# Kernel tuning notes

Measured on AMD Instinct MI355X. Metric: run time of the kernel, lower is better.

Reference implementation:

```python
import jax, jax.numpy as jnp
import numpy as np

B, T, D = 2, 2048, 1024
H, K = 16, 64  # num_heads, key_size (value_size == key_size)


def setup_inputs() -> dict:
    key = jax.random.key(0)
    ks = jax.random.split(key, 9)
    # xavier-uniform-ish scale for square-ish projections
    def xavier(k, shape):
        fan_in, fan_out = shape[0], shape[1]
        lim = jnp.sqrt(6.0 / (fan_in + fan_out))
        return jax.random.uniform(k, shape, jnp.float32, -lim, lim)
    return {
        "x_q": jax.random.normal(ks[0], (B, T, D), jnp.float32),
        "Wq": xavier(ks[1], (D, H * K)),
        "bq": jnp.zeros((H * K,), jnp.float32),
        "Wk": xavier(ks[2], (D, H * K)),
        "bk": jnp.zeros((H * K,), jnp.float32),
        "Wv": xavier(ks[3], (D, H * K)),
        "bv": jnp.zeros((H * K,), jnp.float32),
        "Wo": xavier(ks[4], (H * K, D)),
        "bo": jnp.zeros((D,), jnp.float32),
    }


def reference(x_q, Wq, bq, Wk, bk, Wv, bv, Wo, bo):
    # self-attention: x_k = x_v = x_q
    q = (x_q @ Wq + bq).reshape(B, T, H, K)
    k = (x_q @ Wk + bk).reshape(B, T, H, K)
    v = (x_q @ Wv + bv).reshape(B, T, H, K)
    # dense_dot_product_attention, mask=None
    logits = jnp.einsum('bqhd,bkhd->bhqk', q, k) / jnp.sqrt(jnp.asarray(K, k.dtype))
    attn_w = jax.nn.softmax(logits, axis=-1)  # [B,H,Tq,Tk]
    attn = jnp.einsum('bhqk,bkhd->bqhd', attn_w, v).reshape(B, T, H * K)
    out = attn @ Wo + bo  # [B,T,D]
    return out
```

## Files before the change

kernel.cpp:

```cpp
#include <hip/hip_runtime.h>
#include <hip/hip_bf16.h>
#include <stdint.h>

#define B_  2
#define T_  2048
#define D_  1024
#define H_  16
#define KS  64
#define M_  (B_*T_)

typedef unsigned short u16;
typedef __bf16 bf16x8 __attribute__((ext_vector_type(8)));
typedef __bf16 bf16x4 __attribute__((ext_vector_type(4)));
typedef float  f32x4  __attribute__((ext_vector_type(4)));

#define AS1 __attribute__((address_space(1)))
#define AS3 __attribute__((address_space(3)))

__device__ inline u16 f2bf(float x){
  union { float f; uint32_t u; } v; v.f = x;
  uint32_t r = (v.u + 0x7fffu + ((v.u >> 16) & 1u)) >> 16;
  return (u16)r;
}

__device__ inline void gl_lds16(const u16* g, u16* l){
  __builtin_amdgcn_global_load_lds((AS1 void*)(const_cast<u16*>(g)),
                                   (AS3 void*)l, 16, 0, 0);
}

__global__ __launch_bounds__(256) void k_cvt_x(const float* __restrict__ x,
                                               u16* __restrict__ xb){
  int i = blockIdx.x * 256 + threadIdx.x;
  float4 v = ((const float4*)x)[i];
  ushort4 o;
  o.x = f2bf(v.x); o.y = f2bf(v.y); o.z = f2bf(v.z); o.w = f2bf(v.w);
  ((ushort4*)xb)[i] = o;
}

__global__ __launch_bounds__(256) void k_tconv_w(const float* __restrict__ W0,
                                                 const float* __restrict__ W1,
                                                 const float* __restrict__ W2,
                                                 const float* __restrict__ W3,
                                                 u16* __restrict__ out){
  const float* W = (blockIdx.z==0)?W0:(blockIdx.z==1)?W1:(blockIdx.z==2)?W2:W3;
  u16* o = out + (size_t)blockIdx.z * 1024 * 1024;
  __shared__ float tile[32][33];
  int tx = threadIdx.x, ty = threadIdx.y;
  int kb = blockIdx.y * 32, nb = blockIdx.x * 32;
  for(int i=0;i<4;i++) tile[ty+8*i][tx] = W[(size_t)(kb+ty+8*i)*1024 + nb+tx];
  __syncthreads();
  for(int i=0;i<4;i++){
    int n = nb + ty + 8*i;
    o[(size_t)n*1024 + kb + tx] = f2bf(tile[tx][ty+8*i]);
  }
}

__global__ __launch_bounds__(256) void k_gemm_qkv(const u16* __restrict__ xb,
                                                  const u16* __restrict__ wt,
                                                  const float* __restrict__ bq,
                                                  const float* __restrict__ bk,
                                                  const float* __restrict__ bv,
                                                  u16* __restrict__ qkv){
  int widx = blockIdx.x >> 3;
  int n0   = (blockIdx.x & 7) * 128;
  int m0   = blockIdx.y * 128;
  const u16* BT = wt + (size_t)widx * (1024*1024);
  const float* bias = (widx==0)?bq:(widx==1)?bk:bv;
  u16* out = qkv + (size_t)widx * (4*1024*1024);
  float oscale = (widx==0) ? 0.125f * 1.44269504088896f : 1.0f;

  __shared__ u16 Asm[128*64];
  __shared__ u16 Bsm[128*64];
  int t = threadIdx.x;
  int lane = t & 63, w = t >> 6, wm = w >> 1, wn = w & 1;
  int l15 = lane & 15, l4 = lane >> 4;
  f32x4 zero = {0.f,0.f,0.f,0.f};
  f32x4 acc[4][4];
  for(int i=0;i<4;i++) for(int j=0;j<4;j++) acc[i][j] = zero;
  int srow = t >> 3, schunk = t & 7;

  for(int kt=0; kt<16; ++kt){
    __syncthreads();
    int kb = kt * 64;
    for(int i=0;i<4;i++){
      int row = i*32 + srow;
      int gch = schunk ^ (row & 7);
      gl_lds16(xb + (size_t)(m0+row)*1024 + kb + gch*8, Asm + row*64 + schunk*8);
      gl_lds16(BT + (size_t)(n0+row)*1024 + kb + gch*8, Bsm + row*64 + schunk*8);
    }
    __syncthreads();
    for(int c=0;c<2;c++){
      bf16x8 af[4], bfr[4];
      for(int mt=0;mt<4;mt++){
        int row = wm*64 + mt*16 + l15;
        int idx = (row*64 + c*32 + l4*8) ^ ((row & 7) << 3);
        af[mt] = *(const bf16x8*)(Asm + idx);
      }
      for(int nt=0;nt<4;nt++){
        int row = wn*64 + nt*16 + l15;
        int idx = (row*64 + c*32 + l4*8) ^ ((row & 7) << 3);
        bfr[nt] = *(const bf16x8*)(Bsm + idx);
      }
      for(int mt=0;mt<4;mt++)
        for(int nt=0;nt<4;nt++)
          acc[mt][nt] = __builtin_amdgcn_mfma_f32_16x16x32_bf16(af[mt], bfr[nt], acc[mt][nt], 0,0,0);
    }
  }
  for(int nt=0;nt<4;nt++){
    int nbase = n0 + wn*64 + nt*16 + l15;
    float bv_ = bias[nbase];
    int h = nbase >> 6, kk = nbase & 63;
    for(int mt=0;mt<4;mt++){
      for(int r=0;r<4;r++){
        int m = m0 + wm*64 + mt*16 + l4*4 + r;
        int b = m >> 11, tt = m & 2047;
        out[(((size_t)(b*H_ + h)*T_ + tt) << 6) + kk] = f2bf((acc[mt][nt][r] + bv_) * oscale);
      }
    }
  }
}

__global__ __launch_bounds__(256) void k_tpose_v(const u16* __restrict__ V,
                                                 u16* __restrict__ VT){
  __shared__ u16 tile[64][65];
  int bh = blockIdx.y, tt = blockIdx.x;
  const u16* v = V + ((size_t)bh*T_ + (size_t)tt*64) * 64;
  u16* o = VT + (size_t)bh*64*T_ + (size_t)tt*64;
  int t = threadIdx.x;
  for(int i=0;i<2;i++){
    int r = i*32 + (t>>3); int c0 = (t&7)*8;
    bf16x8 d = *(const bf16x8*)(v + (size_t)r*64 + c0);
    for(int j=0;j<8;j++) tile[r][c0+j] = ((u16*)&d)[j];
  }
  __syncthreads();
  for(int i=0;i<2;i++){
    int d0 = i*32 + (t>>3); int c0 = (t&7)*8;
    union { u16 s[8]; uint4 q; } pk;
    for(int j=0;j<8;j++) pk.s[j] = tile[c0+j][d0];
    *(uint4*)(o + (size_t)d0*T_ + c0) = pk.q;
  }
}

__global__ __launch_bounds__(256) void k_attn(const u16* __restrict__ Q,
                                              const u16* __restrict__ Kg,
                                              const u16* __restrict__ VT,
                                              u16* __restrict__ attn_out){
  int bx = blockIdx.x;
  int qt = bx & 31, h = (bx >> 5) & 15, b = bx >> 9;
  int bh = b*H_ + h;
  const u16* Qh = Q  + (size_t)bh * T_ * 64;
  const u16* Kh = Kg + (size_t)bh * T_ * 64;
  const u16* Vh = VT + (size_t)bh * 64 * T_;
  __shared__ u16 Ksm[2][64*64];
  __shared__ u16 Vsm[2][64*64];
  __shared__ u16 Psm[4][16*64];
  int t = threadIdx.x, lane = t & 63, w = t >> 6;
  int l15 = lane & 15, l4 = lane >> 4;

  bf16x8 qf[2];
  int qrow = qt*64 + w*16 + l15;
  for(int c=0;c<2;c++)
    qf[c] = *(const bf16x8*)(Qh + (size_t)qrow*64 + c*32 + l4*8);

  f32x4 zero = {0.f,0.f,0.f,0.f};
  f32x4 accT[4];
  for(int g=0;g<4;g++) accT[g] = zero;
  float m_r = -3.0e38f, l_r = 0.f;

  int srow = t >> 3, schunk = t & 7;

  for(int i=0;i<2;i++){
    int row = i*32 + srow;
    int gch = schunk ^ (row & 7);
    gl_lds16(Kh + (size_t)row*64 + gch*8,  &Ksm[0][row*64 + schunk*8]);
    gl_lds16(Vh + (size_t)row*T_ + gch*8,  &Vsm[0][row*64 + schunk*8]);
  }
  __syncthreads();

  int cur = 0;
  for(int tile=0; tile<32; ++tile){
    if(tile+1 < 32){
      int kvb = (tile+1)*64;
      for(int i=0;i<2;i++){
        int row = i*32 + srow;
        int gch = schunk ^ (row & 7);
        gl_lds16(Kh + (size_t)(kvb+row)*64 + gch*8, &Ksm[cur^1][row*64 + schunk*8]);
        gl_lds16(Vh + (size_t)row*T_ + kvb + gch*8, &Vsm[cur^1][row*64 + schunk*8]);
      }
    }

    f32x4 s[4];
    for(int g=0;g<4;g++) s[g] = zero;
    __builtin_amdgcn_s_setprio(1);
    for(int c=0;c<2;c++){
      for(int g=0;g<4;g++){
        int row = g*16 + l15;
        int idx = (row*64 + c*32 + l4*8) ^ ((row & 7) << 3);
        bf16x8 kf = *(const bf16x8*)(&Ksm[cur][idx]);
        s[g] = __builtin_amdgcn_mfma_f32_16x16x32_bf16(kf, qf[c], s[g], 0,0,0);
      }
    }
    __builtin_amdgcn_s_setprio(0);

    float pmax = s[0][0];
    for(int g=0;g<4;g++)
      for(int r=0;r<4;r++) pmax = fmaxf(pmax, s[g][r]);
    pmax = fmaxf(pmax, __shfl_xor(pmax, 16));
    pmax = fmaxf(pmax, __shfl_xor(pmax, 32));
    if(__any(pmax > m_r + 8.f)){
      float mnew  = fmaxf(m_r, pmax);
      float alpha = __builtin_amdgcn_exp2f(m_r - mnew);
      m_r = mnew;
      l_r *= alpha;
      for(int g=0;g<4;g++){
        f32x4 a = accT[g];
        for(int r=0;r<4;r++) a[r] *= alpha;
        accT[g] = a;
      }
    }
    float rs = 0.f;
    for(int g=0;g<4;g++)
      for(int r=0;r<4;r++){
        float e = __builtin_amdgcn_exp2f(s[g][r] - m_r);
        s[g][r] = e;
        rs += e;
      }
    rs += __shfl_xor(rs, 16);
    rs += __shfl_xor(rs, 32);
    l_r += rs;

    for(int g=0;g<4;g++){
      bf16x4 pk;
      for(int r=0;r<4;r++) pk[r] = (__bf16)s[g][r];
      int idx = (l15*64 + g*16 + l4*4) ^ ((l15 & 7) << 3);
      *(bf16x4*)(&Psm[w][idx]) = pk;
    }

    __builtin_amdgcn_s_setprio(1);
    for(int c=0;c<2;c++){
      int idx_p = (l15*64 + c*32 + l4*8) ^ ((l15 & 7) << 3);
      bf16x8 pf = *(const bf16x8*)(&Psm[w][idx_p]);
      for(int g=0;g<4;g++){
        int row = g*16 + l15;
        int idx = (row*64 + c*32 + l4*8) ^ ((row & 7) << 3);
        bf16x8 vf = *(const bf16x8*)(&Vsm[cur][idx]);
        accT[g] = __builtin_amdgcn_mfma_f32_16x16x32_bf16(vf, pf, accT[g], 0,0,0);
      }
    }
    __builtin_amdgcn_s_setprio(0);

    __syncthreads();
    cur ^= 1;
  }

  float oinv = 1.0f / l_r;
  int m = b*T_ + qt*64 + w*16 + l15;
  for(int g=0;g<4;g++){
    bf16x4 pk;
    for(int r=0;r<4;r++) pk[r] = (__bf16)(accT[g][r] * oinv);
    *(bf16x4*)(attn_out + (size_t)m*1024 + h*64 + g*16 + l4*4) = pk;
  }
}

__global__ __launch_bounds__(256) void k_gemm_out(const u16* __restrict__ A,
                                                  const u16* __restrict__ BT,
                                                  const float* __restrict__ bias,
                                                  float* __restrict__ out){
  int n0 = blockIdx.x * 128;
  int m0 = blockIdx.y * 64;
  __shared__ u16 Asm[64*64];
  __shared__ u16 Bsm[128*64];
  int t = threadIdx.x;
  int lane = t & 63, w = t >> 6, wm = w >> 1, wn = w & 1;
  int l15 = lane & 15, l4 = lane >> 4;
  f32x4 zero = {0.f,0.f,0.f,0.f};
  f32x4 acc[2][4];
  for(int i=0;i<2;i++) for(int j=0;j<4;j++) acc[i][j] = zero;
  int srow = t >> 3, schunk = t & 7;

  for(int kt=0; kt<16; ++kt){
    __syncthreads();
    int kb = kt * 64;
    for(int i=0;i<2;i++){
      int row = i*32 + srow;
      int gch = schunk ^ (row & 7);
      gl_lds16(A  + (size_t)(m0+row)*1024 + kb + gch*8, Asm + row*64 + schunk*8);
    }
    for(int i=0;i<4;i++){
      int row = i*32 + srow;
      int gch = schunk ^ (row & 7);
      gl_lds16(BT + (size_t)(n0+row)*1024 + kb + gch*8, Bsm + row*64 + schunk*8);
    }
    __syncthreads();
    for(int c=0;c<2;c++){
      bf16x8 af[2], bfr[4];
      for(int mt=0;mt<2;mt++){
        int row = wm*32 + mt*16 + l15;
        int idx = (row*64 + c*32 + l4*8) ^ ((row & 7) << 3);
        af[mt] = *(const bf16x8*)(Asm + idx);
      }
      for(int nt=0;nt<4;nt++){
        int row = wn*64 + nt*16 + l15;
        int idx = (row*64 + c*32 + l4*8) ^ ((row & 7) << 3);
        bfr[nt] = *(const bf16x8*)(Bsm + idx);
      }
      for(int mt=0;mt<2;mt++)
        for(int nt=0;nt<4;nt++)
          acc[mt][nt] = __builtin_amdgcn_mfma_f32_16x16x32_bf16(af[mt], bfr[nt], acc[mt][nt], 0,0,0);
    }
  }
  for(int nt=0;nt<4;nt++){
    int nbase = n0 + wn*64 + nt*16 + l15;
    float bv_ = bias[nbase];
    for(int mt=0;mt<2;mt++){
      for(int r=0;r<4;r++){
        int m = m0 + wm*32 + mt*16 + l4*4 + r;
        out[(size_t)m*1024 + nbase] = acc[mt][nt][r] + bv_;
      }
    }
  }
}

extern "C" void kernel_launch(void* const* d_in, const int* in_sizes, int n_in,
                              void* d_out, int out_size, void* d_ws, size_t ws_size,
                              hipStream_t stream){
  const float* x  = (const float*)d_in[0];
  const float* Wq = (const float*)d_in[1];
  const float* bq = (const float*)d_in[2];
  const float* Wk = (const float*)d_in[3];
  const float* bk = (const float*)d_in[4];
  const float* Wv = (const float*)d_in[5];
  const float* bv = (const float*)d_in[6];
  const float* Wo = (const float*)d_in[7];
  const float* bo = (const float*)d_in[8];
  float* out = (float*)d_out;
  char* ws = (char*)d_ws;

  u16* xb  = (u16*)(ws);
  u16* wt  = (u16*)(ws + (8u  << 20));
  u16* qkv = (u16*)(ws + (16u << 20));
  u16* vt  = (u16*)(ws + (40u << 20));
  u16* at  = (u16*)(ws + (48u << 20));

  k_cvt_x   <<<4096, 256, 0, stream>>>(x, xb);
  k_tconv_w <<<dim3(32,32,4), dim3(32,8), 0, stream>>>(Wq, Wk, Wv, Wo, wt);
  k_gemm_qkv<<<dim3(24,32), 256, 0, stream>>>(xb, wt, bq, bk, bv, qkv);
  k_tpose_v <<<dim3(32,32), 256, 0, stream>>>(qkv + (size_t)8*1024*1024, vt);
  k_attn    <<<1024, 256, 0, stream>>>(qkv, qkv + (size_t)4*1024*1024, vt, at);
  k_gemm_out<<<dim3(8,64), 256, 0, stream>>>(at, wt + (size_t)3*1024*1024, bo, out);
}
```

Before: 219.5 us.

## Fuse V transpose into QKV GEMM epilogue and compute softmax row sums via MFMA

The QKV GEMM now writes V directly in transposed [bh][d][t] layout with 4-wide packed stores, which removes the separate k_tpose_v kernel launch and its extra read and write of V. In the attention kernel, the per-tile row sum of exponentials is computed by an extra MFMA of a ones vector against the P fragment instead of scalar adds plus cross-lane shuffles. The rescaling of the sum moves into the accumulator, and the row max reduction is rebalanced into a tree. Costs are one extra MFMA per chunk, and the sum is taken from bf16-rounded P, which slightly changes numerics.

Measured after the change: 212.8 us. 3.0% less time.

```diff
diff --git a/kernel.cpp b/kernel.cpp
--- a/kernel.cpp
+++ b/kernel.cpp
@@ -60,7 +60,8 @@
                                                   const float* __restrict__ bq,
                                                   const float* __restrict__ bk,
                                                   const float* __restrict__ bv,
-                                                  u16* __restrict__ qkv){
+                                                  u16* __restrict__ qkv,
+                                                  u16* __restrict__ vt){
   int widx = blockIdx.x >> 3;
   int n0   = (blockIdx.x & 7) * 128;
   int m0   = blockIdx.y * 128;
@@ -106,38 +107,32 @@
           acc[mt][nt] = __builtin_amdgcn_mfma_f32_16x16x32_bf16(af[mt], bfr[nt], acc[mt][nt], 0,0,0);
     }
   }
-  for(int nt=0;nt<4;nt++){
-    int nbase = n0 + wn*64 + nt*16 + l15;
-    float bv_ = bias[nbase];
-    int h = nbase >> 6, kk = nbase & 63;
-    for(int mt=0;mt<4;mt++){
-      for(int r=0;r<4;r++){
-        int m = m0 + wm*64 + mt*16 + l4*4 + r;
+  if(widx == 2){
+    for(int nt=0;nt<4;nt++){
+      int nbase = n0 + wn*64 + nt*16 + l15;
+      float bv_ = bias[nbase];
+      int h = nbase >> 6, kk = nbase & 63;
+      for(int mt=0;mt<4;mt++){
+        int m = m0 + wm*64 + mt*16 + l4*4;
         int b = m >> 11, tt = m & 2047;
-        out[(((size_t)(b*H_ + h)*T_ + tt) << 6) + kk] = f2bf((acc[mt][nt][r] + bv_) * oscale);
-      }
-    }
-  }
-}
-
-__global__ __launch_bounds__(256) void k_tpose_v(const u16* __restrict__ V,
-                                                 u16* __restrict__ VT){
-  __shared__ u16 tile[64][65];
-  int bh = blockIdx.y, tt = blockIdx.x;
-  const u16* v = V + ((size_t)bh*T_ + (size_t)tt*64) * 64;
-  u16* o = VT + (size_t)bh*64*T_ + (size_t)tt*64;
-  int t = threadIdx.x;
-  for(int i=0;i<2;i++){
-    int r = i*32 + (t>>3); int c0 = (t&7)*8;
-    bf16x8 d = *(const bf16x8*)(v + (size_t)r*64 + c0);
-    for(int j=0;j<8;j++) tile[r][c0+j] = ((u16*)&d)[j];
-  }
-  __syncthreads();
-  for(int i=0;i<2;i++){
-    int d0 = i*32 + (t>>3); int c0 = (t&7)*8;
-    union { u16 s[8]; uint4 q; } pk;
-    for(int j=0;j<8;j++) pk.s[j] = tile[c0+j][d0];
-    *(uint4*)(o + (size_t)d0*T_ + c0) = pk.q;
+        bf16x4 pk;
+        for(int r=0;r<4;r++) pk[r] = (__bf16)(acc[mt][nt][r] + bv_);
+        *(bf16x4*)(vt + (((size_t)(b*H_ + h)*64 + kk)*T_) + tt) = pk;
+      }
+    }
+  } else {
+    for(int nt=0;nt<4;nt++){
+      int nbase = n0 + wn*64 + nt*16 + l15;
+      float bv_ = bias[nbase];
+      int h = nbase >> 6, kk = nbase & 63;
+      for(int mt=0;mt<4;mt++){
+        for(int r=0;r<4;r++){
+          int m = m0 + wm*64 + mt*16 + l4*4 + r;
+          int b = m >> 11, tt = m & 2047;
+          out[(((size_t)(b*H_ + h)*T_ + tt) << 6) + kk] = f2bf((acc[mt][nt][r] + bv_) * oscale);
+        }
+      }
+    }
   }
 }
 
@@ -162,10 +157,14 @@
   for(int c=0;c<2;c++)
     qf[c] = *(const bf16x8*)(Qh + (size_t)qrow*64 + c*32 + l4*8);
 
+  bf16x8 ones;
+  for(int j=0;j<8;j++) ones[j] = (__bf16)1.0f;
+
   f32x4 zero = {0.f,0.f,0.f,0.f};
   f32x4 accT[4];
   for(int g=0;g<4;g++) accT[g] = zero;
-  float m_r = -3.0e38f, l_r = 0.f;
+  f32x4 accL = zero;
+  float m_r = -3.0e38f;
 
   int srow = t >> 3, schunk = t & 7;
 
@@ -202,32 +201,27 @@
     }
     __builtin_amdgcn_s_setprio(0);
 
-    float pmax = s[0][0];
-    for(int g=0;g<4;g++)
-      for(int r=0;r<4;r++) pmax = fmaxf(pmax, s[g][r]);
+    float t0 = fmaxf(fmaxf(fmaxf(s[0][0], s[0][1]), s[0][2]), s[0][3]);
+    float t1 = fmaxf(fmaxf(fmaxf(s[1][0], s[1][1]), s[1][2]), s[1][3]);
+    float t2 = fmaxf(fmaxf(fmaxf(s[2][0], s[2][1]), s[2][2]), s[2][3]);
+    float t3 = fmaxf(fmaxf(fmaxf(s[3][0], s[3][1]), s[3][2]), s[3][3]);
+    float pmax = fmaxf(fmaxf(fmaxf(t0, t1), t2), t3);
     pmax = fmaxf(pmax, __shfl_xor(pmax, 16));
     pmax = fmaxf(pmax, __shfl_xor(pmax, 32));
     if(__any(pmax > m_r + 8.f)){
       float mnew  = fmaxf(m_r, pmax);
       float alpha = __builtin_amdgcn_exp2f(m_r - mnew);
       m_r = mnew;
-      l_r *= alpha;
       for(int g=0;g<4;g++){
         f32x4 a = accT[g];
         for(int r=0;r<4;r++) a[r] *= alpha;
         accT[g] = a;
       }
-    }
-    float rs = 0.f;
+      for(int r=0;r<4;r++) accL[r] *= alpha;
+    }
     for(int g=0;g<4;g++)
-      for(int r=0;r<4;r++){
-        float e = __builtin_amdgcn_exp2f(s[g][r] - m_r);
-        s[g][r] = e;
-        rs += e;
-      }
-    rs += __shfl_xor(rs, 16);
-    rs += __shfl_xor(rs, 32);
-    l_r += rs;
+      for(int r=0;r<4;r++)
+        s[g][r] = __builtin_amdgcn_exp2f(s[g][r] - m_r);
 
     for(int g=0;g<4;g++){
       bf16x4 pk;
@@ -240,6 +234,7 @@
     for(int c=0;c<2;c++){
       int idx_p = (l15*64 + c*32 + l4*8) ^ ((l15 & 7) << 3);
       bf16x8 pf = *(const bf16x8*)(&Psm[w][idx_p]);
+      accL = __builtin_amdgcn_mfma_f32_16x16x32_bf16(ones, pf, accL, 0,0,0);
       for(int g=0;g<4;g++){
         int row = g*16 + l15;
         int idx = (row*64 + c*32 + l4*8) ^ ((row & 7) << 3);
@@ -253,7 +248,7 @@
     cur ^= 1;
   }
 
-  float oinv = 1.0f / l_r;
+  float oinv = 1.0f / accL[0];
   int m = b*T_ + qt*64 + w*16 + l15;
   for(int g=0;g<4;g++){
     bf16x4 pk;
@@ -344,8 +339,7 @@
 
   k_cvt_x   <<<4096, 256, 0, stream>>>(x, xb);
   k_tconv_w <<<dim3(32,32,4), dim3(32,8), 0, stream>>>(Wq, Wk, Wv, Wo, wt);
-  k_gemm_qkv<<<dim3(24,32), 256, 0, stream>>>(xb, wt, bq, bk, bv, qkv);
-  k_tpose_v <<<dim3(32,32), 256, 0, stream>>>(qkv + (size_t)8*1024*1024, vt);
+  k_gemm_qkv<<<dim3(24,32), 256, 0, stream>>>(xb, wt, bq, bk, bv, qkv, vt);
   k_attn    <<<1024, 256, 0, stream>>>(qkv, qkv + (size_t)4*1024*1024, vt, at);
   k_gemm_out<<<dim3(8,64), 256, 0, stream>>>(at, wt + (size_t)3*1024*1024, bo, out);
 }
```
